# Performance work log

Measured on AMD Instinct MI355X. Metric: run time of the kernel, lower is better.

## Reference

```python
import jax, jax.numpy as jnp
import numpy as np

B, S, D, H = 2, 2048, 768, 12
DEPTH = D // H


def setup_inputs() -> dict:
    key = jax.random.key(0)
    ks = jax.random.split(key, 8)
    scale = 1.0 / np.sqrt(D)
    inp = {
        "query": jax.random.normal(ks[0], (B, S, D), jnp.float32),
        "key": jax.random.normal(ks[1], (B, S, D), jnp.float32),
        "value": jax.random.normal(ks[2], (B, S, D), jnp.float32),
        # additive mask convention: 1.0 where attention is disallowed (causal)
        "mask": jnp.triu(jnp.ones((1, 1, S, S), jnp.float32), k=1),
        "Wq": jax.random.normal(ks[3], (D, D), jnp.float32) * scale,
        "bq": jnp.zeros((D,), jnp.float32),
        "Wk": jax.random.normal(ks[4], (D, D), jnp.float32) * scale,
        "bk": jnp.zeros((D,), jnp.float32),
        "Wv": jax.random.normal(ks[5], (D, D), jnp.float32) * scale,
        "bv": jnp.zeros((D,), jnp.float32),
        "Wo": jax.random.normal(ks[6], (D, D), jnp.float32) * scale,
        "bo": jnp.zeros((D,), jnp.float32),
    }
    return inp


def _split_heads(x):
    # [B, S, D] -> [B, H, S, depth]
    b, s, _ = x.shape
    return x.reshape(b, s, H, DEPTH).transpose(0, 2, 1, 3)


def reference(query, key, value, mask, Wq, bq, Wk, bk, Wv, bv, Wo, bo):
    q = _split_heads(query @ Wq + bq)   # [B,H,S,depth]
    k = _split_heads(key @ Wk + bk)
    v = _split_heads(value @ Wv + bv)

    d_k = jnp.asarray(DEPTH, q.dtype)
    logits = jnp.einsum("bhqd,bhkd->bhqk", q, k) / jnp.sqrt(d_k)
    logits = logits + mask * -1e9
    weights = jax.nn.softmax(logits, axis=-1)          # [B,H,S,S] -- O(N^2)
    attn = jnp.einsum("bhqk,bhkd->bhqd", weights, v)    # [B,H,S,depth]

    concat = attn.transpose(0, 2, 1, 3).reshape(query.shape[0], -1, D)
    return concat @ Wo + bo
```

## Files before the change

kernel.cpp:

```cpp
#include <hip/hip_runtime.h>


typedef __bf16 bf16;
typedef __bf16 bf16x8 __attribute__((ext_vector_type(8)));
typedef __bf16 bf16x4 __attribute__((ext_vector_type(4)));
typedef float  f32x4  __attribute__((ext_vector_type(4)));

__device__ __forceinline__ void async_load16(const void* g, void* l) {
  __builtin_amdgcn_global_load_lds(
      (__attribute__((address_space(1))) void*)g,
      (__attribute__((address_space(3))) void*)l, 16, 0, 0);
}

__constant__ unsigned char chunk_tab[40] = {
  3, 4, 5, 6, 7, 8, 9, 10, 11, 12, 13, 14, 15,
  7 | 16, 8 | 16, 9 | 16, 10 | 16, 11 | 16, 12 | 16, 13 | 16, 14 | 16, 15 | 16,
  11 | 32, 12 | 32, 13 | 32, 14 | 32, 15 | 32,
  15 | 48,
  2, 6 | 16, 10 | 32, 14 | 48,
  1, 5 | 16, 9 | 32, 13 | 48,
  0, 4 | 16, 8 | 32, 12 | 48,
};

__global__ __launch_bounds__(256) void transpose_w_kernel(
    const float* __restrict__ W0, const float* __restrict__ W1,
    const float* __restrict__ W2, const float* __restrict__ W3,
    bf16* __restrict__ T0, bf16* __restrict__ T1,
    bf16* __restrict__ T2, bf16* __restrict__ T3) {
  const float* W; bf16* T;
  switch (blockIdx.z) {
    case 0: W = W0; T = T0; break;
    case 1: W = W1; T = T1; break;
    case 2: W = W2; T = T2; break;
    default: W = W3; T = T3; break;
  }
  __shared__ float tile[32][33];
  const int tx = threadIdx.x, ty = threadIdx.y;
  const int k0 = blockIdx.y * 32, n0 = blockIdx.x * 32;
#pragma unroll
  for (int j = 0; j < 32; j += 8)
    tile[ty + j][tx] = W[(size_t)(k0 + ty + j) * 768 + n0 + tx];
  __syncthreads();
#pragma unroll
  for (int j = 0; j < 32; j += 8) {
    int n = ty + j;
    T[(size_t)(n0 + n) * 768 + k0 + tx] = (bf16)tile[tx][n];
  }
}

__global__ __launch_bounds__(256) void gemm_qkv_kernel(
    const float* __restrict__ X0, const float* __restrict__ X1, const float* __restrict__ X2,
    const bf16* __restrict__ W0, const bf16* __restrict__ W1, const bf16* __restrict__ W2,
    const float* __restrict__ b0, const float* __restrict__ b1, const float* __restrict__ b2,
    bf16* __restrict__ Q, bf16* __restrict__ K, bf16* __restrict__ V) {
  __shared__ __align__(16) char smem[65536];
  const int z = blockIdx.z;
  const float* A   = (z == 0) ? X0 : (z == 1) ? X1 : X2;
  const bf16* Wt   = (z == 0) ? W0 : (z == 1) ? W1 : W2;
  const float* bias = (z == 0) ? b0 : (z == 1) ? b1 : b2;
  bf16* outb = (z == 0) ? Q : (z == 1) ? K : V;
  const int mode = (z == 2) ? 1 : 0;
  const int m0 = blockIdx.y * 128, n0 = blockIdx.x * 128;

  const int t = threadIdx.x;
  const int w = t >> 6, lane = t & 63;
  const int wm = w >> 1, wn = w & 1;
  const int quad = lane >> 4, l15 = lane & 15;
  const int srow = lane >> 3, k8p = lane & 7;

  size_t offB[4]; int ldsOffB[4];
#pragma unroll
  for (int i = 0; i < 4; ++i) {
    const int rl = w * 32 + i * 8 + srow;
    const int kk = k8p ^ (rl & 7);
    offB[i] = (size_t)(n0 + rl) * 768 + kk * 8;
    ldsOffB[i] = (w * 32 + i * 8) * 64;
  }
  const int arow0 = t >> 3;
  const int ac = t & 7;
  size_t offA[4]; int apos[4];
#pragma unroll
  for (int i = 0; i < 4; ++i) {
    const int row = arow0 + i * 32;
    offA[i] = (size_t)(m0 + row) * 768 + ac * 8;
    apos[i] = row * 64 + ((ac ^ (row & 7)) << 3);
  }

  f32x4 acc[4][4] = {};
  f32x4 pa[4], pb[4];

#pragma unroll
  for (int i = 0; i < 4; ++i) {
    pa[i] = *(const f32x4*)(A + offA[i]);
    pb[i] = *(const f32x4*)(A + offA[i] + 4);
  }
#pragma unroll
  for (int i = 0; i < 4; ++i)
    async_load16(Wt + offB[i], smem + 16384 + 2 * ldsOffB[i]);
  {
    bf16* As0 = (bf16*)smem;
#pragma unroll
    for (int i = 0; i < 4; ++i) {
      bf16x8 o;
      o[0]=(bf16)pa[i][0]; o[1]=(bf16)pa[i][1]; o[2]=(bf16)pa[i][2]; o[3]=(bf16)pa[i][3];
      o[4]=(bf16)pb[i][0]; o[5]=(bf16)pb[i][1]; o[6]=(bf16)pb[i][2]; o[7]=(bf16)pb[i][3];
      *(bf16x8*)(As0 + apos[i]) = o;
    }
  }

  for (int kidx = 0; kidx < 12; ++kidx) {
    __syncthreads();
    const int cur = (kidx & 1) * 32768;
    const int nb = ((kidx + 1) & 1) * 32768;
    if (kidx < 11) {
      const int k1 = (kidx + 1) * 64;
#pragma unroll
      for (int i = 0; i < 4; ++i) {
        pa[i] = *(const f32x4*)(A + offA[i] + k1);
        pb[i] = *(const f32x4*)(A + offA[i] + k1 + 4);
      }
#pragma unroll
      for (int i = 0; i < 4; ++i)
        async_load16(Wt + offB[i] + k1, smem + nb + 16384 + 2 * ldsOffB[i]);
    }
    const bf16* As = (const bf16*)(smem + cur);
    const bf16* Bs = (const bf16*)(smem + cur + 16384);
#pragma unroll
    for (int ks = 0; ks < 2; ++ks) {
      bf16x8 af[4], bfv[4];
      const int slot = (((ks * 4 + quad) ^ (lane & 7)) * 8);
#pragma unroll
      for (int mi = 0; mi < 4; ++mi)
        af[mi] = *(const bf16x8*)(As + (wm * 64 + mi * 16 + l15) * 64 + slot);
#pragma unroll
      for (int ni = 0; ni < 4; ++ni)
        bfv[ni] = *(const bf16x8*)(Bs + (wn * 64 + ni * 16 + l15) * 64 + slot);
#pragma unroll
      for (int mi = 0; mi < 4; ++mi)
#pragma unroll
        for (int ni = 0; ni < 4; ++ni)
          acc[mi][ni] = __builtin_amdgcn_mfma_f32_16x16x32_bf16(af[mi], bfv[ni], acc[mi][ni], 0, 0, 0);
    }
    if (kidx < 11) {
      bf16* Asn = (bf16*)(smem + nb);
#pragma unroll
      for (int i = 0; i < 4; ++i) {
        bf16x8 o;
        o[0]=(bf16)pa[i][0]; o[1]=(bf16)pa[i][1]; o[2]=(bf16)pa[i][2]; o[3]=(bf16)pa[i][3];
        o[4]=(bf16)pb[i][0]; o[5]=(bf16)pb[i][1]; o[6]=(bf16)pb[i][2]; o[7]=(bf16)pb[i][3];
        *(bf16x8*)(Asn + apos[i]) = o;
      }
    }
  }

#pragma unroll
  for (int ni = 0; ni < 4; ++ni) {
    const float bc = bias[n0 + wn * 64 + ni * 16 + l15];
#pragma unroll
    for (int mi = 0; mi < 4; ++mi)
#pragma unroll
      for (int r = 0; r < 4; ++r) acc[mi][ni][r] += bc;
  }

  __syncthreads();
  if (mode == 0) {
    bf16* Ce = (bf16*)smem;
#pragma unroll
    for (int ni = 0; ni < 4; ++ni) {
      const int col = wn * 64 + ni * 16 + l15;
#pragma unroll
      for (int mi = 0; mi < 4; ++mi) {
        const int row = wm * 64 + mi * 16 + quad * 4;
#pragma unroll
        for (int r = 0; r < 4; ++r)
          Ce[(row + r) * 136 + col] = (bf16)acc[mi][ni][r];
      }
    }
    __syncthreads();
#pragma unroll
    for (int j = 0; j < 8; ++j) {
      const int ci = j * 256 + t;
      const int row = ci >> 4, c8 = (ci & 15) * 8;
      bf16x8 vv = *(const bf16x8*)(Ce + row * 136 + c8);
      const int rg = m0 + row, cg = n0 + c8;
      const int bb = rg >> 11, s = rg & 2047;
      const int h = cg >> 6, d = cg & 63;
      *(bf16x8*)(outb + ((size_t)(bb * 12 + h) * 2048 + s) * 64 + d) = vv;
    }
  } else {
    bf16* Ct = (bf16*)smem;
#pragma unroll
    for (int ni = 0; ni < 4; ++ni) {
      const int col = wn * 64 + ni * 16 + l15;
#pragma unroll
      for (int mi = 0; mi < 4; ++mi) {
        const int row = wm * 64 + mi * 16 + quad * 4;
        bf16x4 pv;
        pv[0] = (bf16)acc[mi][ni][0]; pv[1] = (bf16)acc[mi][ni][1];
        pv[2] = (bf16)acc[mi][ni][2]; pv[3] = (bf16)acc[mi][ni][3];
        *(bf16x4*)(Ct + (size_t)col * 136 + row) = pv;
      }
    }
    __syncthreads();
#pragma unroll
    for (int j = 0; j < 8; ++j) {
      const int ci = j * 256 + t;
      const int col = ci >> 4, r8 = (ci & 15) * 8;
      bf16x8 vv = *(const bf16x8*)(Ct + col * 136 + r8);
      const int cg = n0 + col;
      const int h = cg >> 6, d = cg & 63;
      const int rg = m0 + r8;
      const int bb = rg >> 11, s = rg & 2047;
      *(bf16x8*)(outb + ((size_t)(bb * 12 + h) * 64 + d) * 2048 + s) = vv;
    }
  }
}

__global__ __launch_bounds__(256) void gemm_out_kernel(
    const bf16* __restrict__ A, const bf16* __restrict__ Wt,
    const float* __restrict__ bias, float* __restrict__ out) {
  __shared__ __align__(16) char smem[65536];
  const int m0 = blockIdx.y * 128, n0 = blockIdx.x * 128;
  const int t = threadIdx.x;
  const int w = t >> 6, lane = t & 63;
  const int wm = w >> 1, wn = w & 1;
  const int quad = lane >> 4, l15 = lane & 15;
  const int srow = lane >> 3, k8p = lane & 7;

  size_t offA[4], offB[4];
  int ldsOff[4];
#pragma unroll
  for (int i = 0; i < 4; ++i) {
    const int rl = w * 32 + i * 8 + srow;
    const int kk = k8p ^ (rl & 7);
    offA[i] = (size_t)(m0 + rl) * 768 + kk * 8;
    offB[i] = (size_t)(n0 + rl) * 768 + kk * 8;
    ldsOff[i] = (w * 32 + i * 8) * 64;
  }

  f32x4 acc[4][4] = {};
#pragma unroll
  for (int i = 0; i < 4; ++i) {
    async_load16(A  + offA[i], smem + 2 * ldsOff[i]);
    async_load16(Wt + offB[i], smem + 16384 + 2 * ldsOff[i]);
  }

  for (int kidx = 0; kidx < 12; ++kidx) {
    __syncthreads();
    if (kidx < 11) {
      const int nb = (kidx + 1) & 1;
      const int k1 = (kidx + 1) * 64;
#pragma unroll
      for (int i = 0; i < 4; ++i) {
        async_load16(A  + offA[i] + k1, smem + nb * 32768 + 2 * ldsOff[i]);
        async_load16(Wt + offB[i] + k1, smem + nb * 32768 + 16384 + 2 * ldsOff[i]);
      }
    }
    const bf16* As = (const bf16*)(smem + (kidx & 1) * 32768);
    const bf16* Bs = (const bf16*)(smem + (kidx & 1) * 32768 + 16384);
#pragma unroll
    for (int ks = 0; ks < 2; ++ks) {
      bf16x8 af[4], bfv[4];
      const int slot = (((ks * 4 + quad) ^ (lane & 7)) * 8);
#pragma unroll
      for (int mi = 0; mi < 4; ++mi)
        af[mi] = *(const bf16x8*)(As + (wm * 64 + mi * 16 + l15) * 64 + slot);
#pragma unroll
      for (int ni = 0; ni < 4; ++ni)
        bfv[ni] = *(const bf16x8*)(Bs + (wn * 64 + ni * 16 + l15) * 64 + slot);
#pragma unroll
      for (int mi = 0; mi < 4; ++mi)
#pragma unroll
        for (int ni = 0; ni < 4; ++ni)
          acc[mi][ni] = __builtin_amdgcn_mfma_f32_16x16x32_bf16(af[mi], bfv[ni], acc[mi][ni], 0, 0, 0);
    }
  }

#pragma unroll
  for (int ni = 0; ni < 4; ++ni) {
    const float bc = bias[n0 + wn * 64 + ni * 16 + l15];
#pragma unroll
    for (int mi = 0; mi < 4; ++mi)
#pragma unroll
      for (int r = 0; r < 4; ++r) acc[mi][ni][r] += bc;
  }

#pragma unroll
  for (int ni = 0; ni < 4; ++ni) {
    const int col = n0 + wn * 64 + ni * 16 + l15;
#pragma unroll
    for (int mi = 0; mi < 4; ++mi) {
      const int row = m0 + wm * 64 + mi * 16 + quad * 4;
#pragma unroll
      for (int r = 0; r < 4; ++r)
        out[(size_t)(row + r) * 768 + col] = acc[mi][ni][r];
    }
  }
}

__global__ __launch_bounds__(256) void attn_kernel(
    const bf16* __restrict__ Qh, const bf16* __restrict__ Kh,
    const bf16* __restrict__ Vt,
    bf16* __restrict__ O0, bf16* __restrict__ O1,
    bf16* __restrict__ O2, bf16* __restrict__ O3,
    float* __restrict__ L0, float* __restrict__ L1,
    float* __restrict__ L2, float* __restrict__ L3) {
  const int ent = chunk_tab[blockIdx.x / 24];
  const int bh = blockIdx.x % 24;
  const int qt = ent & 15, c = ent >> 4;
  const int q0 = qt * 128;
  const int kt_begin = c * 8;
  const int ntiles = 2 * qt + 2;
  const int kt_end = (kt_begin + 8 < ntiles) ? kt_begin + 8 : ntiles;

  __shared__ __align__(16) char smem[49152];
  bf16* Ps = (bf16*)(smem + 32768);

  const int t = threadIdx.x;
  const int w = t >> 6, lane = t & 63, quad = lane >> 4, l15 = lane & 15;
  const int srow = lane >> 3, k8p = lane & 7;
  const bf16* Qp = Qh + (size_t)bh * (2048 * 64);
  const bf16* Kp = Kh + (size_t)bh * (2048 * 64);
  const bf16* Vp = Vt + (size_t)bh * (64 * 2048);

  size_t offK[2], offV[2];
  int ldsOff[2];
#pragma unroll
  for (int i = 0; i < 2; ++i) {
    const int rl = w * 16 + i * 8 + srow;
    const int kk = k8p ^ (rl & 7);
    offK[i] = (size_t)rl * 64 + kk * 8;
    offV[i] = (size_t)rl * 2048 + kk * 8;
    ldsOff[i] = (w * 16 + i * 8) * 64;
  }

  bf16x8 qf[2][2];
#pragma unroll
  for (int mi = 0; mi < 2; ++mi)
#pragma unroll
    for (int ks = 0; ks < 2; ++ks) {
      const int qrow = q0 + w * 32 + mi * 16 + l15;
      qf[mi][ks] = *(const bf16x8*)(Qp + (size_t)qrow * 64 + ks * 32 + quad * 8);
    }

  f32x4 o[2][4] = {};
  float lp[2] = {0.f, 0.f};

  const float sc = 0.125f * 1.44269504f;

#pragma unroll
  for (int i = 0; i < 2; ++i) {
    async_load16(Kp + offK[i] + (size_t)kt_begin * 64 * 64, smem + 2 * ldsOff[i]);
    async_load16(Vp + offV[i] + (size_t)kt_begin * 64,      smem + 8192 + 2 * ldsOff[i]);
  }

  for (int kt = kt_begin; kt < kt_end; ++kt) {
    const int k0 = kt * 64;
    const int cur = kt & 1;
    __syncthreads();
    if (kt + 1 < kt_end) {
      const int nb = cur ^ 1;
#pragma unroll
      for (int i = 0; i < 2; ++i) {
        async_load16(Kp + offK[i] + (size_t)(k0 + 64) * 64, smem + nb * 16384 + 2 * ldsOff[i]);
        async_load16(Vp + offV[i] + (k0 + 64),              smem + nb * 16384 + 8192 + 2 * ldsOff[i]);
      }
    }
    const bf16* Ks = (const bf16*)(smem + cur * 16384);
    const bf16* Vs = (const bf16*)(smem + cur * 16384 + 8192);

    f32x4 st[4][2] = {};
#pragma unroll
    for (int ks = 0; ks < 2; ++ks) {
      const int slot = (((ks * 4 + quad) ^ (lane & 7)) * 8);
      bf16x8 kf[4];
#pragma unroll
      for (int ni = 0; ni < 4; ++ni)
        kf[ni] = *(const bf16x8*)(Ks + (ni * 16 + l15) * 64 + slot);
#pragma unroll
      for (int ni = 0; ni < 4; ++ni)
#pragma unroll
        for (int mi = 0; mi < 2; ++mi)
          st[ni][mi] = __builtin_amdgcn_mfma_f32_16x16x32_bf16(kf[ni], qf[mi][ks], st[ni][mi], 0, 0, 0);
    }

    const bool diag = (k0 + 63 > q0);
#pragma unroll
    for (int mi = 0; mi < 2; ++mi) {
      const int q_local = w * 32 + mi * 16 + l15;
      const int qg = q0 + q_local;
#pragma unroll
      for (int ni = 0; ni < 4; ++ni) {
        bf16x4 pv;
#pragma unroll
        for (int r = 0; r < 4; ++r) {
          float p = __builtin_amdgcn_exp2f(st[ni][mi][r] * sc);
          if (diag && (k0 + ni * 16 + quad * 4 + r > qg)) p = 0.0f;
          lp[mi] += p;
          pv[r] = (bf16)p;
        }
        const int cc = ni * 2 + (quad >> 1);
        *(bf16x4*)(Ps + q_local * 64 + ((cc ^ (q_local & 7)) << 3) + ((quad & 1) << 2)) = pv;
      }
    }

#pragma unroll
    for (int ks = 0; ks < 2; ++ks) {
      const int slot = (((ks * 4 + quad) ^ (lane & 7)) * 8);
      bf16x8 pf[2], vfr[4];
#pragma unroll
      for (int mi = 0; mi < 2; ++mi)
        pf[mi] = *(const bf16x8*)(Ps + (w * 32 + mi * 16 + l15) * 64 + slot);
#pragma unroll
      for (int di = 0; di < 4; ++di)
        vfr[di] = *(const bf16x8*)(Vs + (di * 16 + l15) * 64 + slot);
#pragma unroll
      for (int mi = 0; mi < 2; ++mi)
#pragma unroll
        for (int di = 0; di < 4; ++di)
          o[mi][di] = __builtin_amdgcn_mfma_f32_16x16x32_bf16(pf[mi], vfr[di], o[mi][di], 0, 0, 0);
    }
  }

  bf16* Op; float* Lp_;
  switch (c) {
    case 0: Op = O0; Lp_ = L0; break;
    case 1: Op = O1; Lp_ = L1; break;
    case 2: Op = O2; Lp_ = L2; break;
    default: Op = O3; Lp_ = L3; break;
  }
  const int rows_c = 2048 - 512 * c;
  const size_t rbase = (size_t)bh * rows_c + (q0 - 512 * c);

#pragma unroll
  for (int mi = 0; mi < 2; ++mi) {
    float l = lp[mi];
    l += __shfl_xor(l, 16);
    l += __shfl_xor(l, 32);
    if (quad == 0) Lp_[rbase + w * 32 + mi * 16 + l15] = l;
#pragma unroll
    for (int di = 0; di < 4; ++di) {
      const int d = di * 16 + l15;
#pragma unroll
      for (int r = 0; r < 4; ++r) {
        const size_t row = rbase + w * 32 + mi * 16 + quad * 4 + r;
        Op[row * 64 + d] = (bf16)o[mi][di][r];
      }
    }
  }
}

__global__ __launch_bounds__(256) void combine_kernel(
    const bf16* __restrict__ O0, const bf16* __restrict__ O1,
    const bf16* __restrict__ O2, const bf16* __restrict__ O3,
    const float* __restrict__ L0, const float* __restrict__ L1,
    const float* __restrict__ L2, const float* __restrict__ L3,
    bf16* __restrict__ attb) {
  const int idx = blockIdx.x * 256 + threadIdx.x;
  const int row = idx >> 4;
  const int dd = (idx & 15) << 2;
  const int bh = row >> 11, s = row & 2047;
  float o0, o1, o2, o3;
  {
    bf16x4 v = *(const bf16x4*)(O0 + (size_t)row * 64 + dd);
    o0 = (float)v[0]; o1 = (float)v[1]; o2 = (float)v[2]; o3 = (float)v[3];
  }
  float l = L0[row];
  if (s >= 512) {
    const size_t r1 = (size_t)bh * 1536 + (s - 512);
    bf16x4 v = *(const bf16x4*)(O1 + r1 * 64 + dd);
    o0 += (float)v[0]; o1 += (float)v[1]; o2 += (float)v[2]; o3 += (float)v[3];
    l += L1[r1];
  }
  if (s >= 1024) {
    const size_t r2 = (size_t)bh * 1024 + (s - 1024);
    bf16x4 v = *(const bf16x4*)(O2 + r2 * 64 + dd);
    o0 += (float)v[0]; o1 += (float)v[1]; o2 += (float)v[2]; o3 += (float)v[3];
    l += L2[r2];
  }
  if (s >= 1536) {
    const size_t r3 = (size_t)bh * 512 + (s - 1536);
    bf16x4 v = *(const bf16x4*)(O3 + r3 * 64 + dd);
    o0 += (float)v[0]; o1 += (float)v[1]; o2 += (float)v[2]; o3 += (float)v[3];
    l += L3[r3];
  }
  const float inv = 1.0f / l;
  bf16x4 ov;
  ov[0] = (bf16)(o0 * inv); ov[1] = (bf16)(o1 * inv);
  ov[2] = (bf16)(o2 * inv); ov[3] = (bf16)(o3 * inv);
  const int b = bh / 12, h = bh % 12;
  *(bf16x4*)(attb + ((size_t)(b * 2048 + s)) * 768 + h * 64 + dd) = ov;
}

extern "C" void kernel_launch(void* const* d_in, const int* in_sizes, int n_in,
                              void* d_out, int out_size, void* d_ws, size_t ws_size,
                              hipStream_t stream) {
  const float* query = (const float*)d_in[0];
  const float* key   = (const float*)d_in[1];
  const float* value = (const float*)d_in[2];
  const float* Wq = (const float*)d_in[4];
  const float* bq = (const float*)d_in[5];
  const float* Wk = (const float*)d_in[6];
  const float* bk = (const float*)d_in[7];
  const float* Wv = (const float*)d_in[8];
  const float* bv = (const float*)d_in[9];
  const float* Wo = (const float*)d_in[10];
  const float* bo = (const float*)d_in[11];
  float* out = (float*)d_out;

  char* ws = (char*)d_ws;
  bf16* wtq  = (bf16*)(ws);
  bf16* wtk  = (bf16*)(ws + 1179648);
  bf16* wtv  = (bf16*)(ws + 2359296);
  bf16* wto  = (bf16*)(ws + 3538944);
  bf16* Qh   = (bf16*)(ws + 4718592);
  bf16* Kh   = (bf16*)(ws + 11010048);
  bf16* Vtb  = (bf16*)(ws + 17301504);
  bf16* attb = (bf16*)(ws + 23592960);
  bf16* O0   = (bf16*)(ws + 29884416);
  bf16* O1   = (bf16*)(ws + 36175872);
  bf16* O2   = (bf16*)(ws + 40894464);
  bf16* O3   = (bf16*)(ws + 44040192);
  float* L0  = (float*)(ws + 45613056);
  float* L1  = (float*)(ws + 45809664);
  float* L2  = (float*)(ws + 45957120);
  float* L3  = (float*)(ws + 46055424);

  transpose_w_kernel<<<dim3(24, 24, 4), dim3(32, 8), 0, stream>>>(Wq, Wk, Wv, Wo, wtq, wtk, wtv, wto);
  gemm_qkv_kernel<<<dim3(6, 32, 3), 256, 0, stream>>>(query, key, value, wtq, wtk, wtv, bq, bk, bv, Qh, Kh, Vtb);
  attn_kernel<<<dim3(960), 256, 0, stream>>>(Qh, Kh, Vtb, O0, O1, O2, O3, L0, L1, L2, L3);
  combine_kernel<<<dim3(3072), 256, 0, stream>>>(O0, O1, O2, O3, L0, L1, L2, L3, attb);
  gemm_out_kernel<<<dim3(6, 32), 256, 0, stream>>>(attb, wto, bo, out);
}
```

Baseline: 203.9 us.

## Fuse split-K attention combine into output GEMM and remap blocks per XCD

The combine kernel, which summed the partial attention outputs and normalised them into a bf16 buffer, is removed. The output projection GEMM now loads the partial O chunks directly, sums and scales them by a precomputed inverse row sum, and writes the A tile into LDS itself. A small lsum kernel computes the inverse normalisers. Both GEMMs also use a 1D grid remapped so that consecutive m-tiles land on the same XCD, intended to improve L2 reuse. This removes one full round trip of the intermediate through global memory, but the A loads become synchronous register loads instead of async LDS loads.

```diff
diff --git a/kernel.cpp b/kernel.cpp
--- a/kernel.cpp
+++ b/kernel.cpp
@@ -54,13 +54,18 @@
     const float* __restrict__ b0, const float* __restrict__ b1, const float* __restrict__ b2,
     bf16* __restrict__ Q, bf16* __restrict__ K, bf16* __restrict__ V) {
   __shared__ __align__(16) char smem[65536];
-  const int z = blockIdx.z;
+  const int bidx = blockIdx.x;
+  const int xcd = bidx & 7, ii = bidx >> 3;
+  const int nt = ii % 6, mzi = ii / 6;
+  const int mz = mzi * 8 + xcd;
+  const int m = mz & 31, z = mz >> 5;
+  const int m0 = m * 128, n0 = nt * 128;
+
   const float* A   = (z == 0) ? X0 : (z == 1) ? X1 : X2;
   const bf16* Wt   = (z == 0) ? W0 : (z == 1) ? W1 : W2;
   const float* bias = (z == 0) ? b0 : (z == 1) ? b1 : b2;
   bf16* outb = (z == 0) ? Q : (z == 1) ? K : V;
   const int mode = (z == 2) ? 1 : 0;
-  const int m0 = blockIdx.y * 128, n0 = blockIdx.x * 128;
 
   const int t = threadIdx.x;
   const int w = t >> 6, lane = t & 63;
@@ -212,88 +217,6 @@
       const int rg = m0 + r8;
       const int bb = rg >> 11, s = rg & 2047;
       *(bf16x8*)(outb + ((size_t)(bb * 12 + h) * 64 + d) * 2048 + s) = vv;
-    }
-  }
-}
-
-__global__ __launch_bounds__(256) void gemm_out_kernel(
-    const bf16* __restrict__ A, const bf16* __restrict__ Wt,
-    const float* __restrict__ bias, float* __restrict__ out) {
-  __shared__ __align__(16) char smem[65536];
-  const int m0 = blockIdx.y * 128, n0 = blockIdx.x * 128;
-  const int t = threadIdx.x;
-  const int w = t >> 6, lane = t & 63;
-  const int wm = w >> 1, wn = w & 1;
-  const int quad = lane >> 4, l15 = lane & 15;
-  const int srow = lane >> 3, k8p = lane & 7;
-
-  size_t offA[4], offB[4];
-  int ldsOff[4];
-#pragma unroll
-  for (int i = 0; i < 4; ++i) {
-    const int rl = w * 32 + i * 8 + srow;
-    const int kk = k8p ^ (rl & 7);
-    offA[i] = (size_t)(m0 + rl) * 768 + kk * 8;
-    offB[i] = (size_t)(n0 + rl) * 768 + kk * 8;
-    ldsOff[i] = (w * 32 + i * 8) * 64;
-  }
-
-  f32x4 acc[4][4] = {};
-#pragma unroll
-  for (int i = 0; i < 4; ++i) {
-    async_load16(A  + offA[i], smem + 2 * ldsOff[i]);
-    async_load16(Wt + offB[i], smem + 16384 + 2 * ldsOff[i]);
-  }
-
-  for (int kidx = 0; kidx < 12; ++kidx) {
-    __syncthreads();
-    if (kidx < 11) {
-      const int nb = (kidx + 1) & 1;
-      const int k1 = (kidx + 1) * 64;
-#pragma unroll
-      for (int i = 0; i < 4; ++i) {
-        async_load16(A  + offA[i] + k1, smem + nb * 32768 + 2 * ldsOff[i]);
-        async_load16(Wt + offB[i] + k1, smem + nb * 32768 + 16384 + 2 * ldsOff[i]);
-      }
-    }
-    const bf16* As = (const bf16*)(smem + (kidx & 1) * 32768);
-    const bf16* Bs = (const bf16*)(smem + (kidx & 1) * 32768 + 16384);
-#pragma unroll
-    for (int ks = 0; ks < 2; ++ks) {
-      bf16x8 af[4], bfv[4];
-      const int slot = (((ks * 4 + quad) ^ (lane & 7)) * 8);
-#pragma unroll
-      for (int mi = 0; mi < 4; ++mi)
-        af[mi] = *(const bf16x8*)(As + (wm * 64 + mi * 16 + l15) * 64 + slot);
-#pragma unroll
-      for (int ni = 0; ni < 4; ++ni)
-        bfv[ni] = *(const bf16x8*)(Bs + (wn * 64 + ni * 16 + l15) * 64 + slot);
-#pragma unroll
-      for (int mi = 0; mi < 4; ++mi)
-#pragma unroll
-        for (int ni = 0; ni < 4; ++ni)
-          acc[mi][ni] = __builtin_amdgcn_mfma_f32_16x16x32_bf16(af[mi], bfv[ni], acc[mi][ni], 0, 0, 0);
-    }
-  }
-
-#pragma unroll
-  for (int ni = 0; ni < 4; ++ni) {
-    const float bc = bias[n0 + wn * 64 + ni * 16 + l15];
-#pragma unroll
-    for (int mi = 0; mi < 4; ++mi)
-#pragma unroll
-      for (int r = 0; r < 4; ++r) acc[mi][ni][r] += bc;
-  }
-
-#pragma unroll
-  for (int ni = 0; ni < 4; ++ni) {
-    const int col = n0 + wn * 64 + ni * 16 + l15;
-#pragma unroll
-    for (int mi = 0; mi < 4; ++mi) {
-      const int row = m0 + wm * 64 + mi * 16 + quad * 4;
-#pragma unroll
-      for (int r = 0; r < 4; ++r)
-        out[(size_t)(row + r) * 768 + col] = acc[mi][ni][r];
     }
   }
 }
@@ -345,7 +268,6 @@
 
   f32x4 o[2][4] = {};
   float lp[2] = {0.f, 0.f};
-
   const float sc = 0.125f * 1.44269504f;
 
 #pragma unroll
@@ -450,46 +372,165 @@
   }
 }
 
-__global__ __launch_bounds__(256) void combine_kernel(
+__global__ __launch_bounds__(256) void lsum_kernel(
+    const float* __restrict__ L0, const float* __restrict__ L1,
+    const float* __restrict__ L2, const float* __restrict__ L3,
+    float* __restrict__ Linv) {
+  const int row = blockIdx.x * 256 + threadIdx.x;
+  const int bh = row >> 11, s = row & 2047;
+  float l = L0[row];
+  if (s >= 512)  l += L1[(size_t)bh * 1536 + (s - 512)];
+  if (s >= 1024) l += L2[(size_t)bh * 1024 + (s - 1024)];
+  if (s >= 1536) l += L3[(size_t)bh * 512  + (s - 1536)];
+  Linv[row] = 1.0f / l;
+}
+
+__global__ __launch_bounds__(256) void gemm_out_kernel(
     const bf16* __restrict__ O0, const bf16* __restrict__ O1,
     const bf16* __restrict__ O2, const bf16* __restrict__ O3,
-    const float* __restrict__ L0, const float* __restrict__ L1,
-    const float* __restrict__ L2, const float* __restrict__ L3,
-    bf16* __restrict__ attb) {
-  const int idx = blockIdx.x * 256 + threadIdx.x;
-  const int row = idx >> 4;
-  const int dd = (idx & 15) << 2;
-  const int bh = row >> 11, s = row & 2047;
-  float o0, o1, o2, o3;
-  {
-    bf16x4 v = *(const bf16x4*)(O0 + (size_t)row * 64 + dd);
-    o0 = (float)v[0]; o1 = (float)v[1]; o2 = (float)v[2]; o3 = (float)v[3];
-  }
-  float l = L0[row];
-  if (s >= 512) {
-    const size_t r1 = (size_t)bh * 1536 + (s - 512);
-    bf16x4 v = *(const bf16x4*)(O1 + r1 * 64 + dd);
-    o0 += (float)v[0]; o1 += (float)v[1]; o2 += (float)v[2]; o3 += (float)v[3];
-    l += L1[r1];
-  }
-  if (s >= 1024) {
-    const size_t r2 = (size_t)bh * 1024 + (s - 1024);
-    bf16x4 v = *(const bf16x4*)(O2 + r2 * 64 + dd);
-    o0 += (float)v[0]; o1 += (float)v[1]; o2 += (float)v[2]; o3 += (float)v[3];
-    l += L2[r2];
-  }
-  if (s >= 1536) {
-    const size_t r3 = (size_t)bh * 512 + (s - 1536);
-    bf16x4 v = *(const bf16x4*)(O3 + r3 * 64 + dd);
-    o0 += (float)v[0]; o1 += (float)v[1]; o2 += (float)v[2]; o3 += (float)v[3];
-    l += L3[r3];
-  }
-  const float inv = 1.0f / l;
-  bf16x4 ov;
-  ov[0] = (bf16)(o0 * inv); ov[1] = (bf16)(o1 * inv);
-  ov[2] = (bf16)(o2 * inv); ov[3] = (bf16)(o3 * inv);
-  const int b = bh / 12, h = bh % 12;
-  *(bf16x4*)(attb + ((size_t)(b * 2048 + s)) * 768 + h * 64 + dd) = ov;
+    const float* __restrict__ Linv, const bf16* __restrict__ Wt,
+    const float* __restrict__ bias, float* __restrict__ out) {
+  __shared__ __align__(16) char smem[65536];
+  const int bidx = blockIdx.x;
+  const int xcd = bidx & 7, ii = bidx >> 3;
+  const int nt = ii % 6, mi_ = ii / 6;
+  const int m = mi_ * 8 + xcd;
+  const int m0 = m * 128, n0 = nt * 128;
+  const int bb = m >> 4;
+  const int s0 = (m & 15) * 128;
+  const int nch = 1 + (s0 >= 512) + (s0 >= 1024) + (s0 >= 1536);
+
+  const int t = threadIdx.x;
+  const int w = t >> 6, lane = t & 63;
+  const int wm = w >> 1, wn = w & 1;
+  const int quad = lane >> 4, l15 = lane & 15;
+  const int srow = lane >> 3, k8p = lane & 7;
+
+  size_t offB[4]; int ldsOffB[4];
+#pragma unroll
+  for (int i = 0; i < 4; ++i) {
+    const int rl = w * 32 + i * 8 + srow;
+    const int kk = k8p ^ (rl & 7);
+    offB[i] = (size_t)(n0 + rl) * 768 + kk * 8;
+    ldsOffB[i] = (w * 32 + i * 8) * 64;
+  }
+  const int arow0 = t >> 3;
+  const int ac = t & 7;
+  size_t ro0[4], ro1[4], ro2[4], ro3[4];
+  int lrow[4], apos[4];
+#pragma unroll
+  for (int i = 0; i < 4; ++i) {
+    const int r = arow0 + i * 32;
+    const int s = s0 + r;
+    ro0[i] = (size_t)s * 64 + ac * 8;
+    ro1[i] = (size_t)(s - 512) * 64 + ac * 8;
+    ro2[i] = (size_t)(s - 1024) * 64 + ac * 8;
+    ro3[i] = (size_t)(s - 1536) * 64 + ac * 8;
+    lrow[i] = s;
+    apos[i] = r * 64 + ((ac ^ (r & 7)) << 3);
+  }
+
+  f32x4 acc[4][4] = {};
+  bf16x8 pa0[4], pa1[4], pa2[4], pa3[4];
+  float lv[4];
+
+  auto loadA = [&](int kk) {
+    const size_t bh = (size_t)(bb * 12 + kk);
+#pragma unroll
+    for (int i = 0; i < 4; ++i) {
+      pa0[i] = *(const bf16x8*)(O0 + bh * 131072 + ro0[i]);
+      lv[i] = Linv[bh * 2048 + lrow[i]];
+    }
+    if (nch >= 2)
+#pragma unroll
+      for (int i = 0; i < 4; ++i) pa1[i] = *(const bf16x8*)(O1 + bh * 98304 + ro1[i]);
+    if (nch >= 3)
+#pragma unroll
+      for (int i = 0; i < 4; ++i) pa2[i] = *(const bf16x8*)(O2 + bh * 65536 + ro2[i]);
+    if (nch >= 4)
+#pragma unroll
+      for (int i = 0; i < 4; ++i) pa3[i] = *(const bf16x8*)(O3 + bh * 32768 + ro3[i]);
+  };
+  auto writeA = [&](bf16* As) {
+#pragma unroll
+    for (int i = 0; i < 4; ++i) {
+      float f[8];
+#pragma unroll
+      for (int k = 0; k < 8; ++k) f[k] = (float)pa0[i][k];
+      if (nch >= 2)
+#pragma unroll
+        for (int k = 0; k < 8; ++k) f[k] += (float)pa1[i][k];
+      if (nch >= 3)
+#pragma unroll
+        for (int k = 0; k < 8; ++k) f[k] += (float)pa2[i][k];
+      if (nch >= 4)
+#pragma unroll
+        for (int k = 0; k < 8; ++k) f[k] += (float)pa3[i][k];
+      bf16x8 o;
+#pragma unroll
+      for (int k = 0; k < 8; ++k) o[k] = (bf16)(f[k] * lv[i]);
+      *(bf16x8*)(As + apos[i]) = o;
+    }
+  };
+
+  loadA(0);
+#pragma unroll
+  for (int i = 0; i < 4; ++i)
+    async_load16(Wt + offB[i], smem + 16384 + 2 * ldsOffB[i]);
+  writeA((bf16*)smem);
+
+  for (int kidx = 0; kidx < 12; ++kidx) {
+    __syncthreads();
+    const int cur = (kidx & 1) * 32768;
+    const int nb = ((kidx + 1) & 1) * 32768;
+    if (kidx < 11) {
+      loadA(kidx + 1);
+      const int k1 = (kidx + 1) * 64;
+#pragma unroll
+      for (int i = 0; i < 4; ++i)
+        async_load16(Wt + offB[i] + k1, smem + nb + 16384 + 2 * ldsOffB[i]);
+    }
+    const bf16* As = (const bf16*)(smem + cur);
+    const bf16* Bs = (const bf16*)(smem + cur + 16384);
+#pragma unroll
+    for (int ks = 0; ks < 2; ++ks) {
+      bf16x8 af[4], bfv[4];
+      const int slot = (((ks * 4 + quad) ^ (lane & 7)) * 8);
+#pragma unroll
+      for (int mi = 0; mi < 4; ++mi)
+        af[mi] = *(const bf16x8*)(As + (wm * 64 + mi * 16 + l15) * 64 + slot);
+#pragma unroll
+      for (int ni = 0; ni < 4; ++ni)
+        bfv[ni] = *(const bf16x8*)(Bs + (wn * 64 + ni * 16 + l15) * 64 + slot);
+#pragma unroll
+      for (int mi = 0; mi < 4; ++mi)
+#pragma unroll
+        for (int ni = 0; ni < 4; ++ni)
+          acc[mi][ni] = __builtin_amdgcn_mfma_f32_16x16x32_bf16(af[mi], bfv[ni], acc[mi][ni], 0, 0, 0);
+    }
+    if (kidx < 11) writeA((bf16*)(smem + nb));
+  }
+
+#pragma unroll
+  for (int ni = 0; ni < 4; ++ni) {
+    const float bc = bias[n0 + wn * 64 + ni * 16 + l15];
+#pragma unroll
+    for (int mi = 0; mi < 4; ++mi)
+#pragma unroll
+      for (int r = 0; r < 4; ++r) acc[mi][ni][r] += bc;
+  }
+
+#pragma unroll
+  for (int ni = 0; ni < 4; ++ni) {
+    const int col = n0 + wn * 64 + ni * 16 + l15;
+#pragma unroll
+    for (int mi = 0; mi < 4; ++mi) {
+      const int row = m0 + wm * 64 + mi * 16 + quad * 4;
+#pragma unroll
+      for (int r = 0; r < 4; ++r)
+        out[(size_t)(row + r) * 768 + col] = acc[mi][ni][r];
+    }
+  }
 }
 
 extern "C" void kernel_launch(void* const* d_in, const int* in_sizes, int n_in,
@@ -516,19 +557,19 @@
   bf16* Qh   = (bf16*)(ws + 4718592);
   bf16* Kh   = (bf16*)(ws + 11010048);
   bf16* Vtb  = (bf16*)(ws + 17301504);
-  bf16* attb = (bf16*)(ws + 23592960);
-  bf16* O0   = (bf16*)(ws + 29884416);
-  bf16* O1   = (bf16*)(ws + 36175872);
-  bf16* O2   = (bf16*)(ws + 40894464);
-  bf16* O3   = (bf16*)(ws + 44040192);
-  float* L0  = (float*)(ws + 45613056);
-  float* L1  = (float*)(ws + 45809664);
-  float* L2  = (float*)(ws + 45957120);
-  float* L3  = (float*)(ws + 46055424);
+  bf16* O0   = (bf16*)(ws + 23592960);
+  bf16* O1   = (bf16*)(ws + 29884416);
+  bf16* O2   = (bf16*)(ws + 34603008);
+  bf16* O3   = (bf16*)(ws + 37748736);
+  float* L0  = (float*)(ws + 39321600);
+  float* L1  = (float*)(ws + 39518208);
+  float* L2  = (float*)(ws + 39665664);
+  float* L3  = (float*)(ws + 39763968);
+  float* Liv = (float*)(ws + 39813120);
 
   transpose_w_kernel<<<dim3(24, 24, 4), dim3(32, 8), 0, stream>>>(Wq, Wk, Wv, Wo, wtq, wtk, wtv, wto);
-  gemm_qkv_kernel<<<dim3(6, 32, 3), 256, 0, stream>>>(query, key, value, wtq, wtk, wtv, bq, bk, bv, Qh, Kh, Vtb);
+  gemm_qkv_kernel<<<dim3(576), 256, 0, stream>>>(query, key, value, wtq, wtk, wtv, bq, bk, bv, Qh, Kh, Vtb);
   attn_kernel<<<dim3(960), 256, 0, stream>>>(Qh, Kh, Vtb, O0, O1, O2, O3, L0, L1, L2, L3);
-  combine_kernel<<<dim3(3072), 256, 0, stream>>>(O0, O1, O2, O3, L0, L1, L2, L3, attb);
-  gemm_out_kernel<<<dim3(6, 32), 256, 0, stream>>>(attb, wto, bo, out);
-}
+  lsum_kernel<<<dim3(192), 256, 0, stream>>>(L0, L1, L2, L3, Liv);
+  gemm_out_kernel<<<dim3(192), 256, 0, stream>>>(O0, O1, O2, O3, Liv, wto, bo, out);
+}
```

Result: no change. 204.7 us (+0.4%).
